# Kernel optimization log

Measured on AMD Instinct MI355X. Metric: run time of the kernel, lower is better.

The kernel has to match this reference:

```python
import jax, jax.numpy as jnp
import numpy as np

MARGIN = 1.0


def setup_inputs() -> dict:
    key = jax.random.key(0)
    k1, k2 = jax.random.split(key)
    embeddings = jax.random.normal(k1, (512, 128), dtype=jnp.float32)
    labels = jax.random.randint(k2, (512,), 0, 64)
    return {"embeddings": embeddings, "labels": labels}


def reference(embeddings, labels):
    # embeddings: [B, D], labels: [B]
    B = embeddings.shape[0]

    # Pairwise squared distances, same math as the gathered (a-p)^2 sums:
    # D[i, j] = ||e_i - e_j||^2, shape [B, B]
    diff = embeddings[:, None, :] - embeddings[None, :, :]  # [B, B, D]
    dist = jnp.sum(diff * diff, axis=-1)                    # [B, B]

    # Valid-pair masks (distinct indices; same / different labels).
    diff_index = ~jnp.eye(B, dtype=bool)
    same_label = labels[:, None] == labels[None, :]
    pos_mask = diff_index & same_label    # valid (a, p)
    neg_mask = diff_index & ~same_label   # valid (a, n)

    # Valid triplet mask [a, p, n].
    triplet_mask = pos_mask[:, :, None] & neg_mask[:, None, :]

    # relu(d(a,p) - d(a,n) + margin) over all triplets, mean over valid ones
    # (equivalent to enumerating nonzero mask entries and gathering).
    terms = jax.nn.relu(dist[:, :, None] - dist[:, None, :] + MARGIN)  # [B,B,B]
    loss_sum = jnp.sum(jnp.where(triplet_mask, terms, 0.0))
    count = jnp.sum(triplet_mask).astype(embeddings.dtype)
    return loss_sum / count
```

## Files before the change

kernel.cpp:

```cpp
#include <hip/hip_runtime.h>

#define BATCH 512
#define DIM 128
#define NA 2
#define NBLK (BATCH / NA)
#define NGRP 4
#define GSZ (NBLK / NGRP)
#define NLBL 64
#define MARGIN 1.0f


__global__ __launch_bounds__(256) void triplet_onekernel(
    const float* __restrict__ emb, const int* __restrict__ labels,
    unsigned long long* __restrict__ partial,
    unsigned int* __restrict__ gticket,
    unsigned int* __restrict__ master,
    float* __restrict__ out)
{
    const int b = blockIdx.x;
    const int tid = threadIdx.x;
    const int lane = tid & 63;
    const int wv = tid >> 6;

    __shared__ float ea[NA][DIM];
    __shared__ float drow[NA][BATCH];
    __shared__ float posd[NA][BATCH];
    __shared__ int lbls[BATCH];
    __shared__ int s_np[NA];
    __shared__ float wsum[4];
    __shared__ double dsum[4];
    __shared__ int hist[NLBL];
    __shared__ int s_last;

    for (int j = tid; j < BATCH; j += 256) lbls[j] = labels[j];
    ((float*)ea)[tid] = emb[(size_t)b * NA * DIM + tid];
    __syncthreads();

    int la[NA];
    #pragma unroll
    for (int i = 0; i < NA; ++i) la[i] = lbls[b * NA + i];

    const float4* a0 = reinterpret_cast<const float4*>(ea[0]);
    const float4* a1 = reinterpret_cast<const float4*>(ea[1]);
    for (int j = tid; j < BATCH; j += 256) {
        const float4* ej = reinterpret_cast<const float4*>(emb + (size_t)j * DIM);
        float acc0 = 0.f, acc1 = 0.f;
        #pragma unroll
        for (int d = 0; d < DIM / 4; ++d) {
            float4 v = ej[d];
            float4 x = a0[d];
            float dx = x.x - v.x, dy = x.y - v.y, dz = x.z - v.z, dw = x.w - v.w;
            acc0 += dx * dx + dy * dy + dz * dz + dw * dw;
            float4 y = a1[d];
            dx = y.x - v.x; dy = y.y - v.y; dz = y.z - v.z; dw = y.w - v.w;
            acc1 += dx * dx + dy * dy + dz * dz + dw * dw;
        }
        drow[0][j] = acc0;
        drow[1][j] = acc1;
    }
    __syncthreads();

    if (wv < NA) {
        const int ai = b * NA + wv;
        int np = 0;
        for (int base = 0; base < BATCH; base += 64) {
            int j = base + lane;
            bool pos = (lbls[j] == la[wv]) && (j != ai);
            unsigned long long m = __ballot(pos);
            if (pos) posd[wv][np + __popcll(m & ((1ull << lane) - 1ull))] = drow[wv][j];
            np += __popcll(m);
        }
        if (lane == 0) s_np[wv] = np;
    }
    __syncthreads();

    float lsum = 0.f;
    for (int n = tid; n < BATCH; n += 256) {
        const int ln = lbls[n];
        #pragma unroll
        for (int i = 0; i < NA; ++i) {
            if (ln != la[i]) {
                const float dm = MARGIN - drow[i][n];
                const int np = s_np[i];
                for (int p = 0; p < np; ++p) {
                    float t = posd[i][p] + dm;
                    lsum += (t > 0.f) ? t : 0.f;
                }
            }
        }
    }

    #pragma unroll
    for (int off = 32; off > 0; off >>= 1) lsum += __shfl_down(lsum, off, 64);
    if (lane == 0) wsum[wv] = lsum;
    __syncthreads();

    if (tid == 0) {
        double tot = (double)wsum[0] + (double)wsum[1]
                   + (double)wsum[2] + (double)wsum[3];
        atomicExch(&partial[b], (unsigned long long)__double_as_longlong(tot));
        __threadfence();
        const int g = b >> 6;
        unsigned int prev = atomicAdd(&gticket[g * 64], 1u);
        int fin = 0;
        if (prev == (unsigned)(GSZ - 1) ||
            prev == 0xAAAAAAAAu + (unsigned)(GSZ - 1)) {
            atomicExch(&gticket[g * 64], 0u);
            __threadfence();
            unsigned int mprev = atomicAdd(master, 1u);
            if (mprev == (unsigned)(NGRP - 1) ||
                mprev == 0xAAAAAAAAu + (unsigned)(NGRP - 1)) {
                atomicExch(master, 0u);
                fin = 1;
            }
        }
        s_last = fin;
    }
    __syncthreads();
    if (!s_last) return;

    __threadfence();
    double v = __longlong_as_double(
        (long long)atomicAdd(&partial[tid], 0ull));
    #pragma unroll
    for (int off = 32; off > 0; off >>= 1) v += __shfl_down(v, off, 64);
    if (lane == 0) dsum[wv] = v;

    if (tid < NLBL) hist[tid] = 0;
    __syncthreads();
    for (int j = tid; j < BATCH; j += 256) atomicAdd(&hist[lbls[j]], 1);
    __syncthreads();

    if (wv == 0) {
        long long c = hist[lane];
        long long cnt = c * (c - 1) * ((long long)BATCH - c);
        #pragma unroll
        for (int off = 32; off > 0; off >>= 1) cnt += __shfl_down(cnt, off, 64);
        if (lane == 0) {
            double S = dsum[0] + dsum[1] + dsum[2] + dsum[3];
            out[0] = (float)(S / (double)cnt);
        }
    }
}

extern "C" void kernel_launch(void* const* d_in, const int* in_sizes, int n_in,
                              void* d_out, int out_size, void* d_ws, size_t ws_size,
                              hipStream_t stream) {
    const float* emb = (const float*)d_in[0];
    const int* labels = (const int*)d_in[1];
    float* out = (float*)d_out;

    unsigned int* gticket = (unsigned int*)d_ws;
    unsigned int* master = (unsigned int*)((char*)d_ws + 1024);
    unsigned long long* partial = (unsigned long long*)((char*)d_ws + 4096);

    triplet_onekernel<<<NBLK, 256, 0, stream>>>(emb, labels, partial, gticket,
                                                master, out);
}
```

Baseline: 22.89 us.

## Process four anchors per block and reduce via fixed-point global atomic

Doubles anchors per block from two to four, halving the block count to 128 and reusing each loaded embedding row for four distance computations. All four waves now build positive lists. The per-block partial array plus final 256-element reduction is replaced by a single 64-bit fixed-point atomicAdd accumulator, with poison-value correction on first use. This trades fewer, heavier blocks and less redundant embedding traffic for fixed-point rounding error and contention on one global atomic.

```diff
diff --git a/kernel.cpp b/kernel.cpp
--- a/kernel.cpp
+++ b/kernel.cpp
@@ -2,19 +2,21 @@
 
 #define BATCH 512
 #define DIM 128
-#define NA 2
+#define NA 4
 #define NBLK (BATCH / NA)
-#define NGRP 4
-#define GSZ (NBLK / NGRP)
+#define GSZ 64
+#define NGRP (NBLK / GSZ)
 #define NLBL 64
 #define MARGIN 1.0f
+#define FXSCALE 1048576.0
+#define POISON64 0xAAAAAAAAAAAAAAAAull
 
 
 __global__ __launch_bounds__(256) void triplet_onekernel(
     const float* __restrict__ emb, const int* __restrict__ labels,
-    unsigned long long* __restrict__ partial,
     unsigned int* __restrict__ gticket,
     unsigned int* __restrict__ master,
+    unsigned long long* __restrict__ acc,
     float* __restrict__ out)
 {
     const int b = blockIdx.x;
@@ -28,39 +30,39 @@
     __shared__ int lbls[BATCH];
     __shared__ int s_np[NA];
     __shared__ float wsum[4];
-    __shared__ double dsum[4];
+    __shared__ int s_last, s_poison;
+    __shared__ double s_S;
     __shared__ int hist[NLBL];
-    __shared__ int s_last;
 
     for (int j = tid; j < BATCH; j += 256) lbls[j] = labels[j];
-    ((float*)ea)[tid] = emb[(size_t)b * NA * DIM + tid];
+    for (int k = tid; k < NA * DIM; k += 256)
+        ((float*)ea)[k] = emb[(size_t)b * NA * DIM + k];
     __syncthreads();
 
     int la[NA];
     #pragma unroll
     for (int i = 0; i < NA; ++i) la[i] = lbls[b * NA + i];
 
-    const float4* a0 = reinterpret_cast<const float4*>(ea[0]);
-    const float4* a1 = reinterpret_cast<const float4*>(ea[1]);
     for (int j = tid; j < BATCH; j += 256) {
         const float4* ej = reinterpret_cast<const float4*>(emb + (size_t)j * DIM);
-        float acc0 = 0.f, acc1 = 0.f;
-        #pragma unroll
+        float acc4[NA] = {0.f, 0.f, 0.f, 0.f};
+        #pragma unroll 8
         for (int d = 0; d < DIM / 4; ++d) {
             float4 v = ej[d];
-            float4 x = a0[d];
-            float dx = x.x - v.x, dy = x.y - v.y, dz = x.z - v.z, dw = x.w - v.w;
-            acc0 += dx * dx + dy * dy + dz * dz + dw * dw;
-            float4 y = a1[d];
-            dx = y.x - v.x; dy = y.y - v.y; dz = y.z - v.z; dw = y.w - v.w;
-            acc1 += dx * dx + dy * dy + dz * dz + dw * dw;
+            #pragma unroll
+            for (int i = 0; i < NA; ++i) {
+                float4 x = reinterpret_cast<const float4*>(ea[i])[d];
+                float dx = x.x - v.x, dy = x.y - v.y;
+                float dz = x.z - v.z, dw = x.w - v.w;
+                acc4[i] += dx * dx + dy * dy + dz * dz + dw * dw;
+            }
         }
-        drow[0][j] = acc0;
-        drow[1][j] = acc1;
+        #pragma unroll
+        for (int i = 0; i < NA; ++i) drow[i][j] = acc4[i];
     }
     __syncthreads();
 
-    if (wv < NA) {
+    {
         const int ai = b * NA + wv;
         int np = 0;
         for (int base = 0; base < BATCH; base += 64) {
@@ -98,35 +100,36 @@
     if (tid == 0) {
         double tot = (double)wsum[0] + (double)wsum[1]
                    + (double)wsum[2] + (double)wsum[3];
-        atomicExch(&partial[b], (unsigned long long)__double_as_longlong(tot));
+        atomicAdd(acc, (unsigned long long)llround(tot * FXSCALE));
         __threadfence();
         const int g = b >> 6;
         unsigned int prev = atomicAdd(&gticket[g * 64], 1u);
-        int fin = 0;
+        int fin = 0, poison = 0;
         if (prev == (unsigned)(GSZ - 1) ||
             prev == 0xAAAAAAAAu + (unsigned)(GSZ - 1)) {
             atomicExch(&gticket[g * 64], 0u);
-            __threadfence();
             unsigned int mprev = atomicAdd(master, 1u);
-            if (mprev == (unsigned)(NGRP - 1) ||
-                mprev == 0xAAAAAAAAu + (unsigned)(NGRP - 1)) {
-                atomicExch(master, 0u);
+            if (mprev == (unsigned)(NGRP - 1)) {
                 fin = 1;
+            } else if (mprev == 0xAAAAAAAAu + (unsigned)(NGRP - 1)) {
+                fin = 1; poison = 1;
             }
+            if (fin) atomicExch(master, 0u);
         }
         s_last = fin;
+        s_poison = poison;
     }
     __syncthreads();
     if (!s_last) return;
 
     __threadfence();
-    double v = __longlong_as_double(
-        (long long)atomicAdd(&partial[tid], 0ull));
-    #pragma unroll
-    for (int off = 32; off > 0; off >>= 1) v += __shfl_down(v, off, 64);
-    if (lane == 0) dsum[wv] = v;
-
     if (tid < NLBL) hist[tid] = 0;
+    if (tid == 0) {
+        unsigned long long L = atomicAdd(acc, 0ull);
+        atomicExch(acc, 0ull);
+        if (s_poison) L -= POISON64;
+        s_S = (double)L / FXSCALE;
+    }
     __syncthreads();
     for (int j = tid; j < BATCH; j += 256) atomicAdd(&hist[lbls[j]], 1);
     __syncthreads();
@@ -136,10 +139,7 @@
         long long cnt = c * (c - 1) * ((long long)BATCH - c);
         #pragma unroll
         for (int off = 32; off > 0; off >>= 1) cnt += __shfl_down(cnt, off, 64);
-        if (lane == 0) {
-            double S = dsum[0] + dsum[1] + dsum[2] + dsum[3];
-            out[0] = (float)(S / (double)cnt);
-        }
+        if (lane == 0) out[0] = (float)(s_S / (double)cnt);
     }
 }
 
@@ -152,8 +152,8 @@
 
     unsigned int* gticket = (unsigned int*)d_ws;
     unsigned int* master = (unsigned int*)((char*)d_ws + 1024);
-    unsigned long long* partial = (unsigned long long*)((char*)d_ws + 4096);
+    unsigned long long* acc = (unsigned long long*)((char*)d_ws + 2048);
 
-    triplet_onekernel<<<NBLK, 256, 0, stream>>>(emb, labels, partial, gticket,
-                                                master, out);
+    triplet_onekernel<<<NBLK, 256, 0, stream>>>(emb, labels, gticket, master,
+                                                acc, out);
 }
```

Result: slower. 23.91 us (+4.5%).
